# Performance work log

Hardware: AMD Instinct MI355X
Metric: run time of the kernel (lower is better)

## Reference

```python
import jax, jax.numpy as jnp
import numpy as np

N = 20000          # num_nodes
E = 320000         # num_edges
D = 128            # node_dim
HID = 128          # hidden_dim
OUT = 128          # output_dim
H = 4              # num_heads
C1 = HID // H      # 32, per-head dim layer 0 (concat)
C2 = OUT           # 128, per-head dim last layer (mean over heads)
EPS = 1e-5


def _glorot(k, shape):
    fan_in, fan_out = shape
    s = (6.0 / (fan_in + fan_out)) ** 0.5
    return jax.random.uniform(k, shape, minval=-s, maxval=s, dtype=jnp.float32)


def setup_inputs() -> dict:
    key = jax.random.key(0)
    ks = jax.random.split(key, 24)
    inp = {
        "x": jax.random.normal(ks[0], (N, D), dtype=jnp.float32),
        "edge_index": jax.random.randint(ks[1], (2, E), 0, N, dtype=jnp.int64),
        "W_in": _glorot(ks[2], (D, HID)), "b_in": jnp.zeros((HID,), jnp.float32),
        # layer 0: in=HID, heads*out = H*C1 = HID
        "Wq1": _glorot(ks[3], (HID, H * C1)), "bq1": jnp.zeros((H * C1,), jnp.float32),
        "Wk1": _glorot(ks[4], (HID, H * C1)), "bk1": jnp.zeros((H * C1,), jnp.float32),
        "Wv1": _glorot(ks[5], (HID, H * C1)), "bv1": jnp.zeros((H * C1,), jnp.float32),
        "att1": _glorot(ks[6], (H, 2 * C1)).reshape(1, H, 2 * C1),
        "g1": jnp.ones((HID,), jnp.float32), "beta1": jnp.zeros((HID,), jnp.float32),
        # layer 1 (last): in=HID, heads*out = H*C2
        "Wq2": _glorot(ks[7], (HID, H * C2)), "bq2": jnp.zeros((H * C2,), jnp.float32),
        "Wk2": _glorot(ks[8], (HID, H * C2)), "bk2": jnp.zeros((H * C2,), jnp.float32),
        "Wv2": _glorot(ks[9], (HID, H * C2)), "bv2": jnp.zeros((H * C2,), jnp.float32),
        "att2": _glorot(ks[10], (H, 2 * C2)).reshape(1, H, 2 * C2),
        "g2": jnp.ones((OUT,), jnp.float32), "beta2": jnp.zeros((OUT,), jnp.float32),
        "W_out": _glorot(ks[11], (OUT, OUT)), "b_out": jnp.zeros((OUT,), jnp.float32),
    }
    return inp


def _gat(h, src, dst, Wq, bq, Wk, bk, Wv, bv, att, heads, c):
    # q,k,v: [N, H, C]
    q = (h @ Wq + bq).reshape(-1, heads, c)
    k = (h @ Wk + bk).reshape(-1, heads, c)
    v = (h @ Wv + bv).reshape(-1, heads, c)
    qi = q[dst]            # [E, H, C] target-node query
    kj = k[src]            # [E, H, C] source-node key
    vj = v[src]            # [E, H, C]
    alpha = (jnp.concatenate([qi, kj], axis=-1) * att).sum(-1)  # [E, H]
    # segment softmax over incoming edges of each target node
    m = jax.ops.segment_max(alpha, dst, num_segments=N)         # [N, H]
    ex = jnp.exp(alpha - m[dst])
    s = jax.ops.segment_sum(ex, dst, num_segments=N)            # [N, H]
    a = ex / jnp.maximum(s, 1e-16)[dst]                         # [E, H]
    msg = vj * a[..., None]
    return jax.ops.segment_sum(msg, dst, num_segments=N)        # [N, H, C]


def _ln(x, g, b):
    mu = x.mean(-1, keepdims=True)
    var = ((x - mu) ** 2).mean(-1, keepdims=True)
    return (x - mu) * jax.lax.rsqrt(var + EPS) * g + b


def reference(x, edge_index, W_in, b_in, Wq1, bq1, Wk1, bk1, Wv1, bv1, att1, g1, beta1,
              Wq2, bq2, Wk2, bk2, Wv2, bv2, att2, g2, beta2, W_out, b_out):
    src = edge_index[0]  # source node j
    dst = edge_index[1]  # target node i
    h = jax.nn.relu(x @ W_in + b_in)                               # [N, HID]
    # layer 0: concat heads -> [N, H*C1] = [N, HID], residual, LN, ReLU
    o1 = _gat(h, src, dst, Wq1, bq1, Wk1, bk1, Wv1, bv1, att1, H, C1).reshape(-1, H * C1)
    h = jax.nn.relu(_ln(o1 + h, g1, beta1))
    # layer 1: mean over heads -> [N, OUT], residual (HID==OUT), LN
    o2 = _gat(h, src, dst, Wq2, bq2, Wk2, bk2, Wv2, bv2, att2, H, C2).mean(axis=1)
    h = _ln(o2 + h, g2, beta2)
    z = h @ W_out + b_out                                          # [N, OUT]
    return z
```

## Files before the change

kernel.cpp:

```cpp
#include <hip/hip_runtime.h>
#include <hip/hip_bf16.h>
#include <math.h>

#define N_NODES 20000
#define N_EDGES 320000
#define DIM     128
#define HIDDEN  128
#define NH      4
#define C1      32
#define C2      128
#define VC1     132
#define LN_EPS  1e-5f

__device__ __forceinline__ float wave_sum(float v){
#pragma unroll
  for (int o = 32; o; o >>= 1) v += __shfl_xor(v, o, 64);
  return v;
}
__device__ __forceinline__ float wave_max(float v){
#pragma unroll
  for (int o = 32; o; o >>= 1) v = fmaxf(v, __shfl_xor(v, o, 64));
  return v;
}

__global__ __launch_bounds__(1024) void detect_kernel(const int* __restrict__ ei32,
                                                      int* __restrict__ flag){
  __shared__ int any;
  if (threadIdx.x == 0) any = 0;
  __syncthreads();
  if (ei32[2 * threadIdx.x + 1] != 0) atomicOr(&any, 1);
  __syncthreads();
  if (threadIdx.x == 0) *flag = (any == 0) ? 1 : 0;
}

__global__ void hist_kernel(const int* __restrict__ ei, const int* __restrict__ flag,
                            int* __restrict__ counts){
  const bool wide = (*flag != 0);
  for (int e = blockIdx.x * blockDim.x + threadIdx.x; e < N_EDGES;
       e += gridDim.x * blockDim.x){
    int d = wide ? ei[2 * (N_EDGES + e)] : ei[N_EDGES + e];
    atomicAdd(&counts[d], 1);
  }
}

__global__ __launch_bounds__(1024) void scan_kernel(const int* __restrict__ counts,
    int* __restrict__ row_ptr, int* __restrict__ fill_ptr){
  const int PER = 20;
  int t = threadIdx.x;
  int base = t * PER;
  int local[PER];
  int s = 0;
#pragma unroll
  for (int i = 0; i < PER; i++){
    int idx = base + i;
    int c = (idx < N_NODES) ? counts[idx] : 0;
    s += c; local[i] = s;
  }
  __shared__ int bs[1024];
  bs[t] = s; __syncthreads();
  for (int off = 1; off < 1024; off <<= 1){
    int v = (t >= off) ? bs[t - off] : 0;
    __syncthreads();
    bs[t] += v;
    __syncthreads();
  }
  int excl = bs[t] - s;
  int prev = 0;
#pragma unroll
  for (int i = 0; i < PER; i++){
    int idx = base + i;
    if (idx < N_NODES){
      row_ptr[idx + 1] = excl + local[i];
      fill_ptr[idx]    = excl + prev;
    }
    prev = local[i];
  }
  if (t == 0) row_ptr[0] = 0;
}

__global__ void scatter_kernel(const int* __restrict__ ei, const int* __restrict__ flag,
                               int* __restrict__ fill_ptr, int* __restrict__ col_idx){
  const bool wide = (*flag != 0);
  for (int e = blockIdx.x * blockDim.x + threadIdx.x; e < N_EDGES;
       e += gridDim.x * blockDim.x){
    int d = wide ? ei[2 * (N_EDGES + e)] : ei[N_EDGES + e];
    int s = wide ? ei[2 * e]             : ei[e];
    int pos = atomicAdd(&fill_ptr[d], 1);
    col_idx[pos] = s;
  }
}

__global__ void prep_ak_weights(const float* __restrict__ Wk1, const float* __restrict__ att1,
                                const float* __restrict__ Wk2, const float* __restrict__ att2,
                                float* __restrict__ Wka1, float* __restrict__ Wka2){
  int tid = blockIdx.x * blockDim.x + threadIdx.x;
  int stride = gridDim.x * blockDim.x;
  for (int idx = tid; idx < 128 * NH; idx += stride){
    int k = idx >> 2, h = idx & 3;
    float s = 0.f;
    for (int c = 0; c < C1; c++)
      s += Wk1[k * 128 + h * C1 + c] * att1[h * 2 * C1 + C1 + c];
    Wka1[idx] = s;
  }
  for (int idx = tid; idx < 128 * NH; idx += stride){
    int k = idx >> 2, h = idx & 3;
    float s = 0.f;
    for (int c = 0; c < C2; c++)
      s += Wk2[k * 512 + h * C2 + c] * att2[h * 2 * C2 + C2 + c];
    Wka2[idx] = s;
  }
}

__global__ void prep_w2r(const float* __restrict__ Wv2, const float* __restrict__ bv2,
                         float* __restrict__ W2r, float* __restrict__ mb){
  int tid = blockIdx.x * blockDim.x + threadIdx.x;
  if (tid < 16384){
    int hk = tid >> 5;
    int c4 = (tid & 31) << 2;
    int h = hk >> 7, k = hk & 127;
    *(float4*)&W2r[(size_t)hk * 128 + c4] =
        *(const float4*)&Wv2[(size_t)k * 512 + h * 128 + c4];
  }
  if (tid < 32){
    int c4 = tid << 2;
    float4 b0 = *(const float4*)&bv2[c4];
    float4 b1 = *(const float4*)&bv2[128 + c4];
    float4 b2 = *(const float4*)&bv2[256 + c4];
    float4 b3 = *(const float4*)&bv2[384 + c4];
    *(float4*)&mb[c4] = make_float4(0.25f * (b0.x + b1.x + b2.x + b3.x),
                                    0.25f * (b0.y + b1.y + b2.y + b3.y),
                                    0.25f * (b0.z + b1.z + b2.z + b3.z),
                                    0.25f * (b0.w + b1.w + b2.w + b3.w));
  }
}

__global__ __launch_bounds__(256) void akgemv(const float* __restrict__ hin,
    const float* __restrict__ Wka, float* __restrict__ dst, int V, int VC){
  int wid = threadIdx.x >> 6, lane = threadIdx.x & 63;
  int n = blockIdx.x * 4 + wid;
  if (n >= N_NODES) return;
  float2 hv = *(const float2*)&hin[(size_t)n * 128 + (lane << 1)];
  float4 wa = *(const float4*)&Wka[lane << 3];
  float4 wb = *(const float4*)&Wka[(lane << 3) + 4];
  float p0 = hv.x * wa.x + hv.y * wb.x;
  float p1 = hv.x * wa.y + hv.y * wb.y;
  float p2 = hv.x * wa.z + hv.y * wb.z;
  float p3 = hv.x * wa.w + hv.y * wb.w;
  p0 = wave_sum(p0); p1 = wave_sum(p1); p2 = wave_sum(p2); p3 = wave_sum(p3);
  if (lane == 0)
    *(float4*)&dst[(size_t)n * VC + V] = make_float4(p0, p1, p2, p3);
}

template <int ACT, int K>
__global__ __launch_bounds__(256) void gemm_tile(const float* __restrict__ X,
    const float* __restrict__ W, const float* __restrict__ bias,
    float* __restrict__ Y, int M, int ldY){
  __shared__ float XsT[64][68];
  __shared__ float Ws[64][64];
  const int t = threadIdx.x;
  const int row0 = blockIdx.x * 64;
  const int j0 = blockIdx.y * 64;
  const int ra = (t >> 4) << 2;
  const int cb = (t & 15) << 2;
  float acc[4][4] = {{0.f}};
  for (int k0 = 0; k0 < K; k0 += 64){
    if (k0) __syncthreads();
#pragma unroll
    for (int i = 0; i < 4; i++){
      int idx4 = t + i * 256;
      int r = idx4 >> 4;
      int c4 = (idx4 & 15) << 2;
      int grow = row0 + r; if (grow >= N_NODES) grow = N_NODES - 1;
      float4 v = *(const float4*)&X[(size_t)grow * K + k0 + c4];
      XsT[c4][r] = v.x; XsT[c4 + 1][r] = v.y;
      XsT[c4 + 2][r] = v.z; XsT[c4 + 3][r] = v.w;
    }
#pragma unroll
    for (int i = 0; i < 4; i++){
      int idx4 = t + i * 256;
      int k = idx4 >> 4;
      int c4 = (idx4 & 15) << 2;
      *(float4*)&Ws[k][c4] = *(const float4*)&W[(size_t)(k0 + k) * M + j0 + c4];
    }
    __syncthreads();
#pragma unroll 8
    for (int k = 0; k < 64; k++){
      float4 xv = *(const float4*)&XsT[k][ra];
      float4 wv = *(const float4*)&Ws[k][cb];
      acc[0][0] = fmaf(xv.x, wv.x, acc[0][0]); acc[0][1] = fmaf(xv.x, wv.y, acc[0][1]);
      acc[0][2] = fmaf(xv.x, wv.z, acc[0][2]); acc[0][3] = fmaf(xv.x, wv.w, acc[0][3]);
      acc[1][0] = fmaf(xv.y, wv.x, acc[1][0]); acc[1][1] = fmaf(xv.y, wv.y, acc[1][1]);
      acc[1][2] = fmaf(xv.y, wv.z, acc[1][2]); acc[1][3] = fmaf(xv.y, wv.w, acc[1][3]);
      acc[2][0] = fmaf(xv.z, wv.x, acc[2][0]); acc[2][1] = fmaf(xv.z, wv.y, acc[2][1]);
      acc[2][2] = fmaf(xv.z, wv.z, acc[2][2]); acc[2][3] = fmaf(xv.z, wv.w, acc[2][3]);
      acc[3][0] = fmaf(xv.w, wv.x, acc[3][0]); acc[3][1] = fmaf(xv.w, wv.y, acc[3][1]);
      acc[3][2] = fmaf(xv.w, wv.z, acc[3][2]); acc[3][3] = fmaf(xv.w, wv.w, acc[3][3]);
    }
  }
  const float4 b4 = *(const float4*)&bias[j0 + cb];
#pragma unroll
  for (int i = 0; i < 4; i++){
    int orow = row0 + ra + i;
    if (orow >= N_NODES) break;
    float4 o;
    o.x = acc[i][0] + b4.x; o.y = acc[i][1] + b4.y;
    o.z = acc[i][2] + b4.z; o.w = acc[i][3] + b4.w;
    if (ACT == 1){
      o.x = fmaxf(o.x, 0.f); o.y = fmaxf(o.y, 0.f);
      o.z = fmaxf(o.z, 0.f); o.w = fmaxf(o.w, 0.f);
    }
    *(float4*)&Y[(size_t)orow * ldY + j0 + cb] = o;
  }
}

__global__ __launch_bounds__(256) void gat0(const float* __restrict__ vcat,
    const int* __restrict__ row_ptr, const int* __restrict__ col_idx,
    const float* __restrict__ hres, const float* __restrict__ g,
    const float* __restrict__ beta, float* __restrict__ out){
  __shared__ float exs[4][256];
  int wid = threadIdx.x >> 6;
  int lane = threadIdx.x & 63;
  int n = blockIdx.x * 4 + wid;
  if (n >= N_NODES) return;
  int start = row_ptr[n], end = row_ptr[n + 1];
  float m0 = -1e30f, m1 = -1e30f, m2 = -1e30f, m3 = -1e30f;
  for (int e = start + lane; e < end; e += 64){
    int s = col_idx[e];
    const float4 ak = *(const float4*)&vcat[(size_t)s * VC1 + 128];
    m0 = fmaxf(m0, ak.x); m1 = fmaxf(m1, ak.y);
    m2 = fmaxf(m2, ak.z); m3 = fmaxf(m3, ak.w);
  }
  m0 = wave_max(m0); m1 = wave_max(m1); m2 = wave_max(m2); m3 = wave_max(m3);
  int l5 = lane >> 5;
  int c4 = (lane & 31) << 2;
  int h  = (lane & 31) >> 3;
  float a0 = 0.f, a1 = 0.f, a2 = 0.f, a3 = 0.f;
  float s0 = 0.f, s1 = 0.f, s2 = 0.f, s3 = 0.f;
  for (int base = start; base < end; base += 64){
    int e = base + lane;
    float4 ex = make_float4(0.f, 0.f, 0.f, 0.f);
    int srcj = 0;
    if (e < end){
      srcj = col_idx[e];
      const float4 ak = *(const float4*)&vcat[(size_t)srcj * VC1 + 128];
      ex.x = __expf(ak.x - m0); ex.y = __expf(ak.y - m1);
      ex.z = __expf(ak.z - m2); ex.w = __expf(ak.w - m3);
      s0 += ex.x; s1 += ex.y; s2 += ex.z; s3 += ex.w;
    }
    *(float4*)&exs[wid][lane << 2] = ex;
    __builtin_amdgcn_wave_barrier();
    int cnt = end - base; if (cnt > 64) cnt = 64;
    int half = (cnt + 1) >> 1;
    for (int j = 0; j < half; ++j){
      int jj = 2 * j + l5;
      int jjc = (jj < cnt) ? jj : 0;
      int sj = __shfl(srcj, jjc, 64);
      if (jj < cnt){
        float eh = exs[wid][(jj << 2) + h];
        const float4 v = *(const float4*)&vcat[(size_t)sj * VC1 + c4];
        a0 = fmaf(eh, v.x, a0); a1 = fmaf(eh, v.y, a1);
        a2 = fmaf(eh, v.z, a2); a3 = fmaf(eh, v.w, a3);
      }
    }
    __builtin_amdgcn_wave_barrier();
  }
  a0 += __shfl_xor(a0, 32, 64); a1 += __shfl_xor(a1, 32, 64);
  a2 += __shfl_xor(a2, 32, 64); a3 += __shfl_xor(a3, 32, 64);
  s0 = wave_sum(s0); s1 = wave_sum(s1); s2 = wave_sum(s2); s3 = wave_sum(s3);
  float sh = (h == 0) ? s0 : (h == 1) ? s1 : (h == 2) ? s2 : s3;
  sh = fmaxf(sh, 1e-16f);
  float inv = 1.f / sh;
  const float4 r = *(const float4*)&hres[(size_t)n * HIDDEN + c4];
  float v0 = a0 * inv + r.x, v1 = a1 * inv + r.y;
  float v2 = a2 * inv + r.z, v3 = a3 * inv + r.w;
  float mean = wave_sum(v0 + v1 + v2 + v3) * (1.f / 256.f);
  float d0 = v0 - mean, d1 = v1 - mean, d2 = v2 - mean, d3 = v3 - mean;
  float var = wave_sum(d0*d0 + d1*d1 + d2*d2 + d3*d3) * (1.f / 256.f);
  float rs = rsqrtf(var + LN_EPS);
  const float4 g4 = *(const float4*)&g[c4];
  const float4 b4 = *(const float4*)&beta[c4];
  if (l5 == 0){
    float4 o;
    o.x = fmaxf(d0 * rs * g4.x + b4.x, 0.f);
    o.y = fmaxf(d1 * rs * g4.y + b4.y, 0.f);
    o.z = fmaxf(d2 * rs * g4.z + b4.z, 0.f);
    o.w = fmaxf(d3 * rs * g4.w + b4.w, 0.f);
    *(float4*)&out[(size_t)n * HIDDEN + c4] = o;
  }
}

__global__ __launch_bounds__(256) void gat1_agg(const float* __restrict__ h2,
    const float* __restrict__ ak2,
    const int* __restrict__ row_ptr, const int* __restrict__ col_idx,
    float* __restrict__ u){
  __shared__ float exs[4][256];
  int wid = threadIdx.x >> 6;
  int lane = threadIdx.x & 63;
  int n = blockIdx.x * 4 + wid;
  if (n >= N_NODES) return;
  int start = row_ptr[n], end = row_ptr[n + 1];
  float m0 = -1e30f, m1 = -1e30f, m2 = -1e30f, m3 = -1e30f;
  for (int e = start + lane; e < end; e += 64){
    const float4 a = *(const float4*)&ak2[(size_t)col_idx[e] * 4];
    m0 = fmaxf(m0, a.x); m1 = fmaxf(m1, a.y);
    m2 = fmaxf(m2, a.z); m3 = fmaxf(m3, a.w);
  }
  m0 = wave_max(m0); m1 = wave_max(m1); m2 = wave_max(m2); m3 = wave_max(m3);
  int l5 = lane >> 5;
  int c4 = (lane & 31) << 2;
  float acc[4][4] = {{0.f}};
  float s0 = 0.f, s1 = 0.f, s2 = 0.f, s3 = 0.f;
  for (int base = start; base < end; base += 64){
    int e = base + lane;
    float4 ex = make_float4(0.f, 0.f, 0.f, 0.f);
    int srcj = 0;
    if (e < end){
      srcj = col_idx[e];
      const float4 a = *(const float4*)&ak2[(size_t)srcj * 4];
      ex.x = __expf(a.x - m0); ex.y = __expf(a.y - m1);
      ex.z = __expf(a.z - m2); ex.w = __expf(a.w - m3);
      s0 += ex.x; s1 += ex.y; s2 += ex.z; s3 += ex.w;
    }
    *(float4*)&exs[wid][lane << 2] = ex;
    __builtin_amdgcn_wave_barrier();
    int cnt = end - base; if (cnt > 64) cnt = 64;
    int half = (cnt + 1) >> 1;
    for (int j = 0; j < half; ++j){
      int jj = 2 * j + l5;
      int jjc = (jj < cnt) ? jj : 0;
      int sj = __shfl(srcj, jjc, 64);
      if (jj < cnt){
        const float4 eh = *(const float4*)&exs[wid][jj << 2];
        const float4 v = *(const float4*)&h2[(size_t)sj * 128 + c4];
        acc[0][0] = fmaf(eh.x, v.x, acc[0][0]); acc[0][1] = fmaf(eh.x, v.y, acc[0][1]);
        acc[0][2] = fmaf(eh.x, v.z, acc[0][2]); acc[0][3] = fmaf(eh.x, v.w, acc[0][3]);
        acc[1][0] = fmaf(eh.y, v.x, acc[1][0]); acc[1][1] = fmaf(eh.y, v.y, acc[1][1]);
        acc[1][2] = fmaf(eh.y, v.z, acc[1][2]); acc[1][3] = fmaf(eh.y, v.w, acc[1][3]);
        acc[2][0] = fmaf(eh.z, v.x, acc[2][0]); acc[2][1] = fmaf(eh.z, v.y, acc[2][1]);
        acc[2][2] = fmaf(eh.z, v.z, acc[2][2]); acc[2][3] = fmaf(eh.z, v.w, acc[2][3]);
        acc[3][0] = fmaf(eh.w, v.x, acc[3][0]); acc[3][1] = fmaf(eh.w, v.y, acc[3][1]);
        acc[3][2] = fmaf(eh.w, v.z, acc[3][2]); acc[3][3] = fmaf(eh.w, v.w, acc[3][3]);
      }
    }
    __builtin_amdgcn_wave_barrier();
  }
#pragma unroll
  for (int h = 0; h < 4; h++)
#pragma unroll
    for (int c = 0; c < 4; c++)
      acc[h][c] += __shfl_xor(acc[h][c], 32, 64);
  s0 = wave_sum(s0); s1 = wave_sum(s1); s2 = wave_sum(s2); s3 = wave_sum(s3);
  float w0 = 0.25f / fmaxf(s0, 1e-16f);
  float w1 = 0.25f / fmaxf(s1, 1e-16f);
  float w2 = 0.25f / fmaxf(s2, 1e-16f);
  float w3 = 0.25f / fmaxf(s3, 1e-16f);
  if (l5 == 0){
    float* ur = &u[(size_t)n * 512 + c4];
    *(float4*)(ur)       = make_float4(acc[0][0]*w0, acc[0][1]*w0, acc[0][2]*w0, acc[0][3]*w0);
    *(float4*)(ur + 128) = make_float4(acc[1][0]*w1, acc[1][1]*w1, acc[1][2]*w1, acc[1][3]*w1);
    *(float4*)(ur + 256) = make_float4(acc[2][0]*w2, acc[2][1]*w2, acc[2][2]*w2, acc[2][3]*w2);
    *(float4*)(ur + 384) = make_float4(acc[3][0]*w3, acc[3][1]*w3, acc[3][2]*w3, acc[3][3]*w3);
  }
}

__global__ __launch_bounds__(256) void ln_res(const float* __restrict__ o2,
    const float* hres, const float* __restrict__ g,
    const float* __restrict__ beta, float* out){
  int wid = threadIdx.x >> 6, lane = threadIdx.x & 63;
  int n = blockIdx.x * 4 + wid;
  if (n >= N_NODES) return;
  int c2 = lane << 1;
  float2 a = *(const float2*)&o2[(size_t)n * 128 + c2];
  float2 r = *(const float2*)&hres[(size_t)n * 128 + c2];
  float vx = a.x + r.x, vy = a.y + r.y;
  float mean = wave_sum(vx + vy) * (1.f / 128.f);
  float dx = vx - mean, dy = vy - mean;
  float var = wave_sum(dx * dx + dy * dy) * (1.f / 128.f);
  float rs = rsqrtf(var + LN_EPS);
  float2 gg = *(const float2*)&g[c2];
  float2 bb = *(const float2*)&beta[c2];
  *(float2*)&out[(size_t)n * 128 + c2] =
      make_float2(dx * rs * gg.x + bb.x, dy * rs * gg.y + bb.y);
}

extern "C" void kernel_launch(void* const* d_in, const int* in_sizes, int n_in,
                              void* d_out, int out_size, void* d_ws, size_t ws_size,
                              hipStream_t stream) {
  const float* x     = (const float*)d_in[0];
  const int*   ei    = (const int*)  d_in[1];
  const float* W_in  = (const float*)d_in[2];
  const float* b_in  = (const float*)d_in[3];
  const float* Wk1   = (const float*)d_in[6];
  const float* Wv1   = (const float*)d_in[8];
  const float* bv1   = (const float*)d_in[9];
  const float* att1  = (const float*)d_in[10];
  const float* g1    = (const float*)d_in[11];
  const float* beta1 = (const float*)d_in[12];
  const float* Wk2   = (const float*)d_in[15];
  const float* Wv2   = (const float*)d_in[17];
  const float* bv2   = (const float*)d_in[18];
  const float* att2  = (const float*)d_in[19];
  const float* g2    = (const float*)d_in[20];
  const float* beta2 = (const float*)d_in[21];
  const float* W_out = (const float*)d_in[22];
  const float* b_out = (const float*)d_in[23];
  float* zout = (float*)d_out;

  char* base = (char*)d_ws;
  size_t off = 0;
  auto take = [&](size_t bytes) -> void* {
    void* p = base + off;
    off += (bytes + 255) & ~(size_t)255;
    return p;
  };
  float* h1      = (float*)take((size_t)N_NODES * 128 * 4);
  float* h2      = (float*)take((size_t)N_NODES * 128 * 4);
  float* u       = (float*)take((size_t)N_NODES * 512 * 4);
  float* vcat1   = u;
  float* ak2     = (float*)take((size_t)N_NODES * 4 * 4);
  float* Wka1    = (float*)take(128 * NH * 4);
  float* Wka2    = (float*)take(128 * NH * 4);
  float* W2r     = (float*)take(512 * 128 * 4);
  float* mb      = (float*)take(128 * 4);
  int*   counts  = (int*)take((size_t)N_NODES * 4);
  int*   row_ptr = (int*)take((size_t)(N_NODES + 1) * 4);
  int*   fillp   = (int*)take((size_t)N_NODES * 4);
  int*   col_idx = (int*)take((size_t)N_EDGES * 4);
  int*   eflag   = (int*)take(256);
  float* o2      = h1;
  float* h3      = h2;

  const int RT = (N_NODES + 63) / 64;

  hipMemsetAsync(counts, 0, (size_t)N_NODES * 4, stream);
  detect_kernel<<<1, 1024, 0, stream>>>(ei, eflag);
  hist_kernel<<<512, 256, 0, stream>>>(ei, eflag, counts);
  scan_kernel<<<1, 1024, 0, stream>>>(counts, row_ptr, fillp);
  scatter_kernel<<<512, 256, 0, stream>>>(ei, eflag, fillp, col_idx);

  prep_ak_weights<<<2, 256, 0, stream>>>(Wk1, att1, Wk2, att2, Wka1, Wka2);
  prep_w2r<<<64, 256, 0, stream>>>(Wv2, bv2, W2r, mb);

  gemm_tile<1, 128><<<dim3(RT, 2), 256, 0, stream>>>(x, W_in, b_in, h1, 128, 128);
  gemm_tile<0, 128><<<dim3(RT, 2), 256, 0, stream>>>(h1, Wv1, bv1, vcat1, 128, VC1);
  akgemv<<<(N_NODES + 3) / 4, 256, 0, stream>>>(h1, Wka1, vcat1, 128, VC1);
  gat0<<<N_NODES / 4, 256, 0, stream>>>(vcat1, row_ptr, col_idx, h1, g1, beta1, h2);
  akgemv<<<(N_NODES + 3) / 4, 256, 0, stream>>>(h2, Wka2, ak2, 0, 4);
  gat1_agg<<<N_NODES / 4, 256, 0, stream>>>(h2, ak2, row_ptr, col_idx, u);
  gemm_tile<0, 512><<<dim3(RT, 2), 256, 0, stream>>>(u, W2r, mb, o2, 128, 128);
  ln_res<<<N_NODES / 4, 256, 0, stream>>>(o2, h2, g2, beta2, h3);
  gemm_tile<0, 128><<<dim3(RT, 2), 256, 0, stream>>>(h3, W_out, b_out, zout, 128, 128);
}
```

Before: 363.0 us.

## Replace LDS-tiled GEMM with register-blocked kernel using wave-uniform scalar weight loads

Swaps the shared-memory 64x64 tiled GEMM for a kernel where each lane owns one row and 16 output columns. The weight row is wave-uniform via readfirstlane, so its loads can go through the scalar path and the LDS staging and barriers disappear. X is read per lane with strided scalar loads (row stride K), which gives uncoalesced global access that relies on cache. The intent is to remove LDS traffic and synchronization, at the cost of poorer X access coalescing.

New measurement: 362.6 us. About the same (-0.1%).

```diff
diff --git a/kernel.cpp b/kernel.cpp
--- a/kernel.cpp
+++ b/kernel.cpp
@@ -152,64 +152,49 @@
 }
 
 template <int ACT, int K>
-__global__ __launch_bounds__(256) void gemm_tile(const float* __restrict__ X,
+__global__ __launch_bounds__(256) void gemm_sb(const float* __restrict__ X,
     const float* __restrict__ W, const float* __restrict__ bias,
     float* __restrict__ Y, int M, int ldY){
-  __shared__ float XsT[64][68];
-  __shared__ float Ws[64][64];
-  const int t = threadIdx.x;
-  const int row0 = blockIdx.x * 64;
-  const int j0 = blockIdx.y * 64;
-  const int ra = (t >> 4) << 2;
-  const int cb = (t & 15) << 2;
-  float acc[4][4] = {{0.f}};
-  for (int k0 = 0; k0 < K; k0 += 64){
-    if (k0) __syncthreads();
-#pragma unroll
-    for (int i = 0; i < 4; i++){
-      int idx4 = t + i * 256;
-      int r = idx4 >> 4;
-      int c4 = (idx4 & 15) << 2;
-      int grow = row0 + r; if (grow >= N_NODES) grow = N_NODES - 1;
-      float4 v = *(const float4*)&X[(size_t)grow * K + k0 + c4];
-      XsT[c4][r] = v.x; XsT[c4 + 1][r] = v.y;
-      XsT[c4 + 2][r] = v.z; XsT[c4 + 3][r] = v.w;
-    }
-#pragma unroll
-    for (int i = 0; i < 4; i++){
-      int idx4 = t + i * 256;
-      int k = idx4 >> 4;
-      int c4 = (idx4 & 15) << 2;
-      *(float4*)&Ws[k][c4] = *(const float4*)&W[(size_t)(k0 + k) * M + j0 + c4];
-    }
-    __syncthreads();
-#pragma unroll 8
-    for (int k = 0; k < 64; k++){
-      float4 xv = *(const float4*)&XsT[k][ra];
-      float4 wv = *(const float4*)&Ws[k][cb];
-      acc[0][0] = fmaf(xv.x, wv.x, acc[0][0]); acc[0][1] = fmaf(xv.x, wv.y, acc[0][1]);
-      acc[0][2] = fmaf(xv.x, wv.z, acc[0][2]); acc[0][3] = fmaf(xv.x, wv.w, acc[0][3]);
-      acc[1][0] = fmaf(xv.y, wv.x, acc[1][0]); acc[1][1] = fmaf(xv.y, wv.y, acc[1][1]);
-      acc[1][2] = fmaf(xv.y, wv.z, acc[1][2]); acc[1][3] = fmaf(xv.y, wv.w, acc[1][3]);
-      acc[2][0] = fmaf(xv.z, wv.x, acc[2][0]); acc[2][1] = fmaf(xv.z, wv.y, acc[2][1]);
-      acc[2][2] = fmaf(xv.z, wv.z, acc[2][2]); acc[2][3] = fmaf(xv.z, wv.w, acc[2][3]);
-      acc[3][0] = fmaf(xv.w, wv.x, acc[3][0]); acc[3][1] = fmaf(xv.w, wv.y, acc[3][1]);
-      acc[3][2] = fmaf(xv.w, wv.z, acc[3][2]); acc[3][3] = fmaf(xv.w, wv.w, acc[3][3]);
-    }
-  }
-  const float4 b4 = *(const float4*)&bias[j0 + cb];
-#pragma unroll
-  for (int i = 0; i < 4; i++){
-    int orow = row0 + ra + i;
-    if (orow >= N_NODES) break;
-    float4 o;
-    o.x = acc[i][0] + b4.x; o.y = acc[i][1] + b4.y;
-    o.z = acc[i][2] + b4.z; o.w = acc[i][3] + b4.w;
-    if (ACT == 1){
-      o.x = fmaxf(o.x, 0.f); o.y = fmaxf(o.y, 0.f);
-      o.z = fmaxf(o.z, 0.f); o.w = fmaxf(o.w, 0.f);
-    }
-    *(float4*)&Y[(size_t)orow * ldY + j0 + cb] = o;
+  const int lane = threadIdx.x & 63;
+  const int col0 = __builtin_amdgcn_readfirstlane(
+      blockIdx.y * 64 + ((threadIdx.x >> 6) << 4));
+  const int row = blockIdx.x * 64 + lane;
+  int rclamp = row < N_NODES ? row : N_NODES - 1;
+  const float* xr = X + (size_t)rclamp * K;
+  float acc[16];
+#pragma unroll
+  for (int c = 0; c < 16; c++) acc[c] = 0.f;
+#pragma unroll 4
+  for (int k = 0; k < K; ++k){
+    float xv = xr[k];
+    const float* wr = W + (size_t)k * M + col0;
+    float4 wa = *(const float4*)(wr);
+    float4 wb = *(const float4*)(wr + 4);
+    float4 wc = *(const float4*)(wr + 8);
+    float4 wd = *(const float4*)(wr + 12);
+    acc[0]  = fmaf(xv, wa.x, acc[0]);  acc[1]  = fmaf(xv, wa.y, acc[1]);
+    acc[2]  = fmaf(xv, wa.z, acc[2]);  acc[3]  = fmaf(xv, wa.w, acc[3]);
+    acc[4]  = fmaf(xv, wb.x, acc[4]);  acc[5]  = fmaf(xv, wb.y, acc[5]);
+    acc[6]  = fmaf(xv, wb.z, acc[6]);  acc[7]  = fmaf(xv, wb.w, acc[7]);
+    acc[8]  = fmaf(xv, wc.x, acc[8]);  acc[9]  = fmaf(xv, wc.y, acc[9]);
+    acc[10] = fmaf(xv, wc.z, acc[10]); acc[11] = fmaf(xv, wc.w, acc[11]);
+    acc[12] = fmaf(xv, wd.x, acc[12]); acc[13] = fmaf(xv, wd.y, acc[13]);
+    acc[14] = fmaf(xv, wd.z, acc[14]); acc[15] = fmaf(xv, wd.w, acc[15]);
+  }
+  if (row < N_NODES){
+    float* yr = Y + (size_t)row * ldY + col0;
+#pragma unroll
+    for (int j = 0; j < 4; j++){
+      float4 b4 = *(const float4*)&bias[col0 + 4 * j];
+      float4 o;
+      o.x = acc[4*j]     + b4.x; o.y = acc[4*j + 1] + b4.y;
+      o.z = acc[4*j + 2] + b4.z; o.w = acc[4*j + 3] + b4.w;
+      if (ACT == 1){
+        o.x = fmaxf(o.x, 0.f); o.y = fmaxf(o.y, 0.f);
+        o.z = fmaxf(o.z, 0.f); o.w = fmaxf(o.w, 0.f);
+      }
+      *(float4*)(yr + 4 * j) = o;
+    }
   }
 }
 
@@ -441,13 +426,13 @@
   prep_ak_weights<<<2, 256, 0, stream>>>(Wk1, att1, Wk2, att2, Wka1, Wka2);
   prep_w2r<<<64, 256, 0, stream>>>(Wv2, bv2, W2r, mb);
 
-  gemm_tile<1, 128><<<dim3(RT, 2), 256, 0, stream>>>(x, W_in, b_in, h1, 128, 128);
-  gemm_tile<0, 128><<<dim3(RT, 2), 256, 0, stream>>>(h1, Wv1, bv1, vcat1, 128, VC1);
+  gemm_sb<1, 128><<<dim3(RT, 2), 256, 0, stream>>>(x, W_in, b_in, h1, 128, 128);
+  gemm_sb<0, 128><<<dim3(RT, 2), 256, 0, stream>>>(h1, Wv1, bv1, vcat1, 128, VC1);
   akgemv<<<(N_NODES + 3) / 4, 256, 0, stream>>>(h1, Wka1, vcat1, 128, VC1);
   gat0<<<N_NODES / 4, 256, 0, stream>>>(vcat1, row_ptr, col_idx, h1, g1, beta1, h2);
   akgemv<<<(N_NODES + 3) / 4, 256, 0, stream>>>(h2, Wka2, ak2, 0, 4);
   gat1_agg<<<N_NODES / 4, 256, 0, stream>>>(h2, ak2, row_ptr, col_idx, u);
-  gemm_tile<0, 512><<<dim3(RT, 2), 256, 0, stream>>>(u, W2r, mb, o2, 128, 128);
+  gemm_sb<0, 512><<<dim3(RT, 2), 256, 0, stream>>>(u, W2r, mb, o2, 128, 128);
   ln_res<<<N_NODES / 4, 256, 0, stream>>>(o2, h2, g2, beta2, h3);
-  gemm_tile<0, 128><<<dim3(RT, 2), 256, 0, stream>>>(h3, W_out, b_out, zout, 128, 128);
-}
+  gemm_sb<0, 128><<<dim3(RT, 2), 256, 0, stream>>>(h3, W_out, b_out, zout, 128, 128);
+}
```
